# Kernel optimization log

Hardware: AMD Instinct MI355X
Metric: run time of the kernel (lower is better)

Reference implementation:

```python
import jax, jax.numpy as jnp
import numpy as np

NUM_HEADS = 16

def setup_inputs() -> dict:
    key = jax.random.key(0)
    ks = jax.random.split(key, 7)
    D = 1024
    B, S = 8, 1024
    s = 0.02
    return {
        "x": jax.random.normal(ks[0], (B, S, D), dtype=jnp.float32),
        "Wq": jax.random.normal(ks[1], (D, D), dtype=jnp.float32) * s,
        "bq": jnp.zeros((D,), dtype=jnp.float32),
        "Wk": jax.random.normal(ks[2], (D, D), dtype=jnp.float32) * s,
        "bk": jnp.zeros((D,), dtype=jnp.float32),
        "Wv": jax.random.normal(ks[3], (D, D), dtype=jnp.float32) * s,
        "bv": jnp.zeros((D,), dtype=jnp.float32),
    }

def reference(x, Wq, bq, Wk, bk, Wv, bv):
    B, S, D = x.shape
    H = NUM_HEADS
    hd = D // H
    scale = hd ** 0.5
    # projections (torch Linear: x @ W.T + b); weights here stored as [D, D] acting as W.T already
    q = (x @ Wq + bq).reshape(B, S, H, hd).transpose(0, 2, 1, 3)  # [B,H,S,hd]
    k = (x @ Wk + bk).reshape(B, S, H, hd).transpose(0, 2, 1, 3)
    v = (x @ Wv + bv).reshape(B, S, H, hd).transpose(0, 2, 1, 3)
    scores = jnp.einsum("bhqd,bhkd->bhqk", q, k) / scale
    attn_weights = jax.nn.softmax(scores, axis=-1)
    # dropout p=0.0 -> identity; out_prok is never applied in the source forward
    attn = jnp.einsum("bhqk,bhkd->bhqd", attn_weights, v)
    attn = attn.transpose(0, 2, 1, 3).reshape(B, S, D)
    return (attn, attn_weights)
```

## Files before the change

kernel.cpp:

```cpp
#include <hip/hip_runtime.h>
#include <hip/hip_bf16.h>

typedef __attribute__((ext_vector_type(8))) short short8;
typedef __attribute__((ext_vector_type(4))) float f32x4;


__device__ __forceinline__ void gload16(const void* g, void* l) {
  __builtin_amdgcn_global_load_lds((const __attribute__((address_space(1))) void*)g,
                                   (__attribute__((address_space(3))) void*)l, 16, 0, 0);
}

__device__ __forceinline__ short f2bf(float x) {
  __hip_bfloat16 h = __float2bfloat16(x);
  return __builtin_bit_cast(short, h);
}

__global__ void k_conv_x(const float* __restrict__ X, __hip_bfloat16* __restrict__ Xb) {
  int i = (blockIdx.x * 256 + threadIdx.x) * 4;
  float4 v = *(const float4*)(X + i);
  __hip_bfloat16 t[4];
  t[0] = __float2bfloat16(v.x); t[1] = __float2bfloat16(v.y);
  t[2] = __float2bfloat16(v.z); t[3] = __float2bfloat16(v.w);
  *(uint2*)(Xb + i) = *(uint2*)t;
}

__global__ void k_transpose_w(const float* __restrict__ Wq, const float* __restrict__ Wk,
                              const float* __restrict__ Wv, __hip_bfloat16* __restrict__ Wt) {
  __shared__ float t[32][33];
  const int w = blockIdx.z;
  const float* W = (w == 0) ? Wq : ((w == 1) ? Wk : Wv);
  const int k0 = blockIdx.x * 32, n0 = blockIdx.y * 32;
  const int tx = threadIdx.x, ty = threadIdx.y;
  #pragma unroll
  for (int i = 0; i < 4; ++i)
    t[ty + i * 8][tx] = W[(size_t)(k0 + ty + i * 8) * 1024 + n0 + tx];
  __syncthreads();
  __hip_bfloat16* o = Wt + (size_t)w * 1024 * 1024;
  #pragma unroll
  for (int i = 0; i < 4; ++i)
    o[(size_t)(n0 + ty + i * 8) * 1024 + k0 + tx] = __float2bfloat16(t[tx][ty + i * 8]);
}

__global__ __launch_bounds__(256) void k_qkv_gemm(
    const __hip_bfloat16* __restrict__ Xb,
    const __hip_bfloat16* __restrict__ Wt,
    const float* __restrict__ bq, const float* __restrict__ bk, const float* __restrict__ bv,
    __hip_bfloat16* __restrict__ Out)
{
  __shared__ __hip_bfloat16 lA[128 * 64];
  __shared__ __hip_bfloat16 lB[128 * 64];
  const int tid = threadIdx.x;
  const int wv = tid >> 6, lane = tid & 63;
  const int m0 = blockIdx.x * 128;
  const int n0 = blockIdx.y * 128;
  const int wm = wv >> 1, wn = wv & 1;

  f32x4 acc[4][4];
  #pragma unroll
  for (int i = 0; i < 4; ++i)
    #pragma unroll
    for (int j = 0; j < 4; ++j) acc[i][j] = (f32x4)0.0f;

  const int srow = lane >> 3;
  const int scol = (lane & 7) * 8;

  for (int kt = 0; kt < 16; ++kt) {
    const __hip_bfloat16* gA = Xb + (size_t)m0 * 1024 + kt * 64;
    const __hip_bfloat16* gB = Wt + (size_t)n0 * 1024 + kt * 64;
    #pragma unroll
    for (int i = 0; i < 4; ++i) {
      int r0 = wv * 32 + i * 8;
      gload16(gA + (size_t)(r0 + srow) * 1024 + scol, &lA[r0 * 64]);
      gload16(gB + (size_t)(r0 + srow) * 1024 + scol, &lB[r0 * 64]);
    }
    __syncthreads();
    #pragma unroll
    for (int ks = 0; ks < 2; ++ks) {
      short8 af[4], bfr[4];
      #pragma unroll
      for (int mi = 0; mi < 4; ++mi)
        af[mi] = *(const short8*)&lA[(wm * 64 + mi * 16 + (lane & 15)) * 64 + ks * 32 + (lane >> 4) * 8];
      #pragma unroll
      for (int ni = 0; ni < 4; ++ni)
        bfr[ni] = *(const short8*)&lB[(wn * 64 + ni * 16 + (lane & 15)) * 64 + ks * 32 + (lane >> 4) * 8];
      #pragma unroll
      for (int mi = 0; mi < 4; ++mi)
        #pragma unroll
        for (int ni = 0; ni < 4; ++ni)
          acc[mi][ni] = __builtin_amdgcn_mfma_f32_16x16x32_bf16(af[mi], bfr[ni], acc[mi][ni], 0, 0, 0);
    }
    __syncthreads();
  }

  const int which = n0 >> 10;
  const float* bias = (which == 0) ? bq : ((which == 1) ? bk : bv);
  __hip_bfloat16* O = Out + (size_t)which * (8192ull * 1024);
  #pragma unroll
  for (int ni = 0; ni < 4; ++ni) {
    int col = (n0 & 1023) + wn * 64 + ni * 16 + (lane & 15);
    float bb = bias[col];
    #pragma unroll
    for (int mi = 0; mi < 4; ++mi) {
      int rowb = m0 + wm * 64 + mi * 16 + (lane >> 4) * 4;
      #pragma unroll
      for (int r = 0; r < 4; ++r)
        O[(size_t)(rowb + r) * 1024 + col] = __float2bfloat16(acc[mi][ni][r] + bb);
    }
  }
}

__global__ void k_transpose_v(const __hip_bfloat16* __restrict__ V, __hip_bfloat16* __restrict__ Vt) {
  __shared__ __hip_bfloat16 t[32][33];
  const int bh = blockIdx.z, b = bh >> 4, h = bh & 15;
  const int s0 = blockIdx.x * 32, d0 = blockIdx.y * 32;
  const int tx = threadIdx.x, ty = threadIdx.y;
  const __hip_bfloat16* Vb = V + ((size_t)b * 1024) * 1024 + h * 64;
  #pragma unroll
  for (int i = 0; i < 4; ++i)
    t[ty + i * 8][tx] = Vb[(size_t)(s0 + ty + i * 8) * 1024 + d0 + tx];
  __syncthreads();
  __hip_bfloat16* o = Vt + ((size_t)bh * 64 + d0) * 1024 + s0;
  #pragma unroll
  for (int i = 0; i < 4; ++i)
    o[(size_t)(ty + i * 8) * 1024 + tx] = t[tx][ty + i * 8];
}

__global__ __launch_bounds__(256) void k_attn(
    const __hip_bfloat16* __restrict__ Qb,
    const __hip_bfloat16* __restrict__ Kb,
    const __hip_bfloat16* __restrict__ Vt,
    float* __restrict__ attn,
    float* __restrict__ aw)
{
  __shared__ __hip_bfloat16 lK[128 * 64];
  __shared__ float lS[64 * 128];
  const int tid = threadIdx.x;
  const int wv = tid >> 6, lane = tid & 63;
  const int ln15 = lane & 15, lnhi = lane >> 4;
  const int bh = blockIdx.y, b = bh >> 4, h = bh & 15;
  const int q0 = blockIdx.x * 64;
  const size_t head_off = ((size_t)b * 1024) * 1024 + h * 64;
  const float C = 0.18033688f;

  short8 qf[2];
  {
    const __hip_bfloat16* qrow =
        Qb + head_off + (size_t)(q0 + wv * 16 + ln15) * 1024 + lnhi * 8;
    qf[0] = *(const short8*)qrow;
    qf[1] = *(const short8*)(qrow + 32);
  }

  float m2[4], l_run[4];
  #pragma unroll
  for (int r = 0; r < 4; ++r) { m2[r] = -3.0e38f; l_run[r] = 0.0f; }

  const int ksrow = lane >> 3, kchk = lane & 7;

  for (int kt = 0; kt < 8; ++kt) {
    const __hip_bfloat16* gK = Kb + head_off + (size_t)(kt * 128) * 1024;
    #pragma unroll
    for (int i = 0; i < 4; ++i) {
      int r0 = wv * 32 + i * 8;
      int row = r0 + ksrow;
      gload16(gK + (size_t)row * 1024 + ((kchk ^ (row & 7)) << 3), &lK[r0 * 64]);
    }
    __syncthreads();
    f32x4 s[8];
    #pragma unroll
    for (int ni = 0; ni < 8; ++ni) s[ni] = (f32x4)0.0f;
    __builtin_amdgcn_s_setprio(1);
    #pragma unroll
    for (int ks = 0; ks < 2; ++ks) {
      #pragma unroll
      for (int ni = 0; ni < 8; ++ni) {
        int R = ni * 16 + ln15;
        short8 kf = *(const short8*)&lK[R * 64 + (((ks * 4 + lnhi) ^ (R & 7)) << 3)];
        s[ni] = __builtin_amdgcn_mfma_f32_16x16x32_bf16(qf[ks], kf, s[ni], 0, 0, 0);
      }
    }
    __builtin_amdgcn_s_setprio(0);
    __syncthreads();
    #pragma unroll
    for (int r = 0; r < 4; ++r) {
      float mt = -3.0e38f;
      #pragma unroll
      for (int ni = 0; ni < 8; ++ni) mt = fmaxf(mt, s[ni][r]);
      float mt2 = mt * C;
      #pragma unroll
      for (int off = 1; off < 16; off <<= 1) mt2 = fmaxf(mt2, __shfl_xor(mt2, off, 64));
      float mnew = fmaxf(m2[r], mt2);
      float sum = 0.0f;
      #pragma unroll
      for (int ni = 0; ni < 8; ++ni) sum += exp2f(fmaf(s[ni][r], C, -mnew));
      #pragma unroll
      for (int off = 1; off < 16; off <<= 1) sum += __shfl_xor(sum, off, 64);
      l_run[r] = l_run[r] * exp2f(m2[r] - mnew) + sum;
      m2[r] = mnew;
    }
  }

  float c2[4];
  #pragma unroll
  for (int r = 0; r < 4; ++r) c2[r] = m2[r] + __log2f(l_run[r]);

  f32x4 o[4];
  #pragma unroll
  for (int ni = 0; ni < 4; ++ni) o[ni] = (f32x4)0.0f;

  const int rl = wv * 16 + lnhi * 4;

  for (int kt = 0; kt < 8; ++kt) {
    const __hip_bfloat16* gK = Kb + head_off + (size_t)(kt * 128) * 1024;
    #pragma unroll
    for (int i = 0; i < 4; ++i) {
      int r0 = wv * 32 + i * 8;
      int row = r0 + ksrow;
      gload16(gK + (size_t)row * 1024 + ((kchk ^ (row & 7)) << 3), &lK[r0 * 64]);
    }
    __syncthreads();
    f32x4 s[8];
    #pragma unroll
    for (int ni = 0; ni < 8; ++ni) s[ni] = (f32x4)0.0f;
    __builtin_amdgcn_s_setprio(1);
    #pragma unroll
    for (int ks = 0; ks < 2; ++ks) {
      #pragma unroll
      for (int ni = 0; ni < 8; ++ni) {
        int R = ni * 16 + ln15;
        short8 kf = *(const short8*)&lK[R * 64 + (((ks * 4 + lnhi) ^ (R & 7)) << 3)];
        s[ni] = __builtin_amdgcn_mfma_f32_16x16x32_bf16(qf[ks], kf, s[ni], 0, 0, 0);
      }
    }
    __builtin_amdgcn_s_setprio(0);
    #pragma unroll
    for (int ni = 0; ni < 8; ++ni) {
      int c = ni * 16 + ln15;
      #pragma unroll
      for (int r = 0; r < 4; ++r) {
        int row = rl + r;
        float p = exp2f(fmaf(s[ni][r], C, -c2[r]));
        *(float*)((char*)lS + (((row << 9) + (c << 2)) ^ ((row & 7) << 4))) = p;
      }
    }
    __syncthreads();
    const __hip_bfloat16* gV = Vt + (size_t)bh * (64ull * 1024) + kt * 128;
    #pragma unroll
    for (int i = 0; i < 4; ++i) {
      int r0 = wv * 16 + i * 4;
      int row = r0 + lnhi;
      gload16(gV + (size_t)row * 1024 + ((ln15 ^ (row & 7)) << 3), &lK[r0 * 128]);
    }
    float* awb = aw + (size_t)bh * (1024ull * 1024) + (size_t)q0 * 1024 + kt * 128;
    #pragma unroll
    for (int i = 0; i < 8; ++i) {
      int idx = i * 256 + tid;
      int row = idx >> 5, ch = idx & 31;
      f32x4 v = *(const f32x4*)((const char*)lS + ((row << 9) + ((ch ^ (row & 7)) << 4)));
      *(f32x4*)(awb + (size_t)row * 1024 + ch * 4) = v;
    }
    __syncthreads();
    __builtin_amdgcn_s_setprio(1);
    #pragma unroll
    for (int ks = 0; ks < 4; ++ks) {
      int R = wv * 16 + ln15;
      int c0 = ks * 8 + lnhi * 2;
      const char* bp = (const char*)lS + (R << 9);
      f32x4 pa = *(const f32x4*)(bp + ((c0 ^ (R & 7)) << 4));
      f32x4 pb = *(const f32x4*)(bp + (((c0 + 1) ^ (R & 7)) << 4));
      short8 pf;
      pf[0] = f2bf(pa[0]); pf[1] = f2bf(pa[1]); pf[2] = f2bf(pa[2]); pf[3] = f2bf(pa[3]);
      pf[4] = f2bf(pb[0]); pf[5] = f2bf(pb[1]); pf[6] = f2bf(pb[2]); pf[7] = f2bf(pb[3]);
      #pragma unroll
      for (int ni = 0; ni < 4; ++ni) {
        int Rv = ni * 16 + ln15;
        short8 vf = *(const short8*)&lK[Rv * 128 + (((ks * 4 + lnhi) ^ (Rv & 7)) << 3)];
        o[ni] = __builtin_amdgcn_mfma_f32_16x16x32_bf16(pf, vf, o[ni], 0, 0, 0);
      }
    }
    __builtin_amdgcn_s_setprio(0);
    __syncthreads();
  }

  #pragma unroll
  for (int ni = 0; ni < 4; ++ni) {
    int c = h * 64 + ni * 16 + ln15;
    #pragma unroll
    for (int r = 0; r < 4; ++r)
      attn[((size_t)b * 1024 + q0 + rl + r) * 1024 + c] = o[ni][r];
  }
}

extern "C" void kernel_launch(void* const* d_in, const int* in_sizes, int n_in,
                              void* d_out, int out_size, void* d_ws, size_t ws_size,
                              hipStream_t stream) {
  const float* x  = (const float*)d_in[0];
  const float* Wq = (const float*)d_in[1];
  const float* bq = (const float*)d_in[2];
  const float* Wk = (const float*)d_in[3];
  const float* bk = (const float*)d_in[4];
  const float* Wv = (const float*)d_in[5];
  const float* bv = (const float*)d_in[6];
  float* attn = (float*)d_out;
  float* aw   = (float*)d_out + 8ull * 1024 * 1024;

  char* ws = (char*)d_ws;
  __hip_bfloat16* Xb  = (__hip_bfloat16*)(ws);
  __hip_bfloat16* Wt  = (__hip_bfloat16*)(ws + (16ull << 20));
  __hip_bfloat16* QKV = (__hip_bfloat16*)(ws + (22ull << 20));
  __hip_bfloat16* Vt  = (__hip_bfloat16*)(ws + (70ull << 20));
  __hip_bfloat16* Qb = QKV;
  __hip_bfloat16* Kb = QKV + 8ull * 1024 * 1024;
  __hip_bfloat16* Vb = QKV + 16ull * 1024 * 1024;

  k_conv_x<<<8192, 256, 0, stream>>>(x, Xb);
  k_transpose_w<<<dim3(32, 32, 3), dim3(32, 8), 0, stream>>>(Wq, Wk, Wv, Wt);
  k_qkv_gemm<<<dim3(64, 24), 256, 0, stream>>>(Xb, Wt, bq, bk, bv, QKV);
  k_transpose_v<<<dim3(32, 2, 128), dim3(32, 8), 0, stream>>>(Vb, Vt);
  k_attn<<<dim3(16, 128), 256, 0, stream>>>(Qb, Kb, Vt, attn, aw);
}
```

Before: 813.4 us.

## Load K/V fragments directly from global, use per-wave LDS, and remap blocks across XCDs

Drops the shared K/V LDS staging and all block-wide barriers in the attention kernel. Each wave now reads its K and V MFMA fragments straight from global memory (through the caches) and keeps its probability tile in a private LDS slice. Block IDs are also remapped so that blocks of the same head land on the same XCD, which should improve L2 reuse of K and V. The trade-off is redundant global loads across the four waves and unswizzled scattered 16-byte reads, in exchange for removing synchronization and LDS traffic.

```diff
diff --git a/kernel.cpp b/kernel.cpp
--- a/kernel.cpp
+++ b/kernel.cpp
@@ -132,13 +132,16 @@
     float* __restrict__ attn,
     float* __restrict__ aw)
 {
-  __shared__ __hip_bfloat16 lK[128 * 64];
   __shared__ float lS[64 * 128];
   const int tid = threadIdx.x;
   const int wv = tid >> 6, lane = tid & 63;
   const int ln15 = lane & 15, lnhi = lane >> 4;
-  const int bh = blockIdx.y, b = bh >> 4, h = bh & 15;
-  const int q0 = blockIdx.x * 64;
+
+  const int id = blockIdx.x + (blockIdx.y << 4);
+  const int xcd = id & 7, j = id >> 3;
+  const int q0 = (j >> 4) * 64;
+  const int bh = ((j & 15) << 3) | xcd;
+  const int b = bh >> 4, h = bh & 15;
   const size_t head_off = ((size_t)b * 1024) * 1024 + h * 64;
   const float C = 0.18033688f;
 
@@ -150,21 +153,14 @@
     qf[1] = *(const short8*)(qrow + 32);
   }
 
+  const __hip_bfloat16* kfb = Kb + head_off + (size_t)ln15 * 1024 + (lnhi << 3);
+  const __hip_bfloat16* vfb = Vt + (size_t)bh * (64ull * 1024) + (size_t)ln15 * 1024 + (lnhi << 3);
+
   float m2[4], l_run[4];
   #pragma unroll
   for (int r = 0; r < 4; ++r) { m2[r] = -3.0e38f; l_run[r] = 0.0f; }
 
-  const int ksrow = lane >> 3, kchk = lane & 7;
-
   for (int kt = 0; kt < 8; ++kt) {
-    const __hip_bfloat16* gK = Kb + head_off + (size_t)(kt * 128) * 1024;
-    #pragma unroll
-    for (int i = 0; i < 4; ++i) {
-      int r0 = wv * 32 + i * 8;
-      int row = r0 + ksrow;
-      gload16(gK + (size_t)row * 1024 + ((kchk ^ (row & 7)) << 3), &lK[r0 * 64]);
-    }
-    __syncthreads();
     f32x4 s[8];
     #pragma unroll
     for (int ni = 0; ni < 8; ++ni) s[ni] = (f32x4)0.0f;
@@ -173,13 +169,11 @@
     for (int ks = 0; ks < 2; ++ks) {
       #pragma unroll
       for (int ni = 0; ni < 8; ++ni) {
-        int R = ni * 16 + ln15;
-        short8 kf = *(const short8*)&lK[R * 64 + (((ks * 4 + lnhi) ^ (R & 7)) << 3)];
+        short8 kf = *(const short8*)(kfb + (size_t)((kt << 7) + (ni << 4)) * 1024 + (ks << 5));
         s[ni] = __builtin_amdgcn_mfma_f32_16x16x32_bf16(qf[ks], kf, s[ni], 0, 0, 0);
       }
     }
     __builtin_amdgcn_s_setprio(0);
-    __syncthreads();
     #pragma unroll
     for (int r = 0; r < 4; ++r) {
       float mt = -3.0e38f;
@@ -207,17 +201,9 @@
   #pragma unroll
   for (int ni = 0; ni < 4; ++ni) o[ni] = (f32x4)0.0f;
 
-  const int rl = wv * 16 + lnhi * 4;
+  char* ws_ = (char*)(lS + wv * 2048);
 
   for (int kt = 0; kt < 8; ++kt) {
-    const __hip_bfloat16* gK = Kb + head_off + (size_t)(kt * 128) * 1024;
-    #pragma unroll
-    for (int i = 0; i < 4; ++i) {
-      int r0 = wv * 32 + i * 8;
-      int row = r0 + ksrow;
-      gload16(gK + (size_t)row * 1024 + ((kchk ^ (row & 7)) << 3), &lK[r0 * 64]);
-    }
-    __syncthreads();
     f32x4 s[8];
     #pragma unroll
     for (int ni = 0; ni < 8; ++ni) s[ni] = (f32x4)0.0f;
@@ -226,8 +212,7 @@
     for (int ks = 0; ks < 2; ++ks) {
       #pragma unroll
       for (int ni = 0; ni < 8; ++ni) {
-        int R = ni * 16 + ln15;
-        short8 kf = *(const short8*)&lK[R * 64 + (((ks * 4 + lnhi) ^ (R & 7)) << 3)];
+        short8 kf = *(const short8*)(kfb + (size_t)((kt << 7) + (ni << 4)) * 1024 + (ks << 5));
         s[ni] = __builtin_amdgcn_mfma_f32_16x16x32_bf16(qf[ks], kf, s[ni], 0, 0, 0);
       }
     }
@@ -237,50 +222,39 @@
       int c = ni * 16 + ln15;
       #pragma unroll
       for (int r = 0; r < 4; ++r) {
-        int row = rl + r;
+        int lrow = lnhi * 4 + r;
         float p = exp2f(fmaf(s[ni][r], C, -c2[r]));
-        *(float*)((char*)lS + (((row << 9) + (c << 2)) ^ ((row & 7) << 4))) = p;
-      }
-    }
-    __syncthreads();
-    const __hip_bfloat16* gV = Vt + (size_t)bh * (64ull * 1024) + kt * 128;
-    #pragma unroll
-    for (int i = 0; i < 4; ++i) {
-      int r0 = wv * 16 + i * 4;
-      int row = r0 + lnhi;
-      gload16(gV + (size_t)row * 1024 + ((ln15 ^ (row & 7)) << 3), &lK[r0 * 128]);
-    }
-    float* awb = aw + (size_t)bh * (1024ull * 1024) + (size_t)q0 * 1024 + kt * 128;
+        *(float*)(ws_ + (((lrow << 9) + (c << 2)) ^ ((lrow & 7) << 4))) = p;
+      }
+    }
+    float* awb = aw + (size_t)bh * (1024ull * 1024) + (size_t)(q0 + wv * 16) * 1024 + kt * 128;
     #pragma unroll
     for (int i = 0; i < 8; ++i) {
-      int idx = i * 256 + tid;
-      int row = idx >> 5, ch = idx & 31;
-      f32x4 v = *(const f32x4*)((const char*)lS + ((row << 9) + ((ch ^ (row & 7)) << 4)));
-      *(f32x4*)(awb + (size_t)row * 1024 + ch * 4) = v;
-    }
-    __syncthreads();
+      int idx = i * 64 + lane;
+      int lrow = idx >> 5, ch = idx & 31;
+      f32x4 v = *(const f32x4*)(ws_ + ((lrow << 9) + ((ch ^ (lrow & 7)) << 4)));
+      *(f32x4*)(awb + (size_t)lrow * 1024 + ch * 4) = v;
+    }
     __builtin_amdgcn_s_setprio(1);
     #pragma unroll
     for (int ks = 0; ks < 4; ++ks) {
-      int R = wv * 16 + ln15;
       int c0 = ks * 8 + lnhi * 2;
-      const char* bp = (const char*)lS + (R << 9);
-      f32x4 pa = *(const f32x4*)(bp + ((c0 ^ (R & 7)) << 4));
-      f32x4 pb = *(const f32x4*)(bp + (((c0 + 1) ^ (R & 7)) << 4));
+      const char* bp = ws_ + (ln15 << 9);
+      f32x4 pa = *(const f32x4*)(bp + ((c0 ^ (ln15 & 7)) << 4));
+      f32x4 pb = *(const f32x4*)(bp + (((c0 + 1) ^ (ln15 & 7)) << 4));
       short8 pf;
       pf[0] = f2bf(pa[0]); pf[1] = f2bf(pa[1]); pf[2] = f2bf(pa[2]); pf[3] = f2bf(pa[3]);
       pf[4] = f2bf(pb[0]); pf[5] = f2bf(pb[1]); pf[6] = f2bf(pb[2]); pf[7] = f2bf(pb[3]);
       #pragma unroll
       for (int ni = 0; ni < 4; ++ni) {
-        int Rv = ni * 16 + ln15;
-        short8 vf = *(const short8*)&lK[Rv * 128 + (((ks * 4 + lnhi) ^ (Rv & 7)) << 3)];
+        short8 vf = *(const short8*)(vfb + (size_t)(ni << 4) * 1024 + (kt << 7) + (ks << 5));
         o[ni] = __builtin_amdgcn_mfma_f32_16x16x32_bf16(pf, vf, o[ni], 0, 0, 0);
       }
     }
     __builtin_amdgcn_s_setprio(0);
-    __syncthreads();
-  }
-
+  }
+
+  const int rl = wv * 16 + lnhi * 4;
   #pragma unroll
   for (int ni = 0; ni < 4; ++ni) {
     int c = h * 64 + ni * 16 + ln15;
```

Result: slower. 1.003 ms (+23.3%).
